# Optimization experiments

Hardware: AMD Instinct MI355X
Metric: run time of the kernel (lower is better)

## Reference

```python
import jax, jax.numpy as jnp
import numpy as np

WS = 2
D = 128  # hidden_dim per direction
SCALE_X = float(np.sqrt(2.0))  # rescale=True, highway_bias=0 -> sqrt(1+exp(0))


def sru_bidir(x, W, wc, b, k):
    """Bidirectional single-layer SRU (sru lib, layer_norm=False, rescale=True).
    x: (L, N, din). Returns (L, N, 2*D)."""
    L, N, _ = x.shape
    U = (x @ W).reshape(L, N, 2, D, k)  # (L,N,dir,D,k)
    vf, vr = wc.reshape(2, 2, D)  # each (dir, D)
    bf, br = b.reshape(2, 2, D)
    # time-reverse the backward direction so one scan handles both
    U = jnp.concatenate([U[:, :, :1], U[::-1, :, 1:]], axis=2)
    if k == 4:
        xprime = U[..., 3]
    else:
        xp = x.reshape(L, N, 2, D)
        xprime = jnp.concatenate([xp[:, :, :1], xp[::-1, :, 1:]], axis=2) * SCALE_X

    def step(c, inp):
        u0, u1, u2, xpt = inp  # each (N,2,D)
        f = jax.nn.sigmoid(u1 + vf * c + bf)
        c = f * c + (1.0 - f) * u0
        r = jax.nn.sigmoid(u2 + vr * c + br)
        h = r * c + (1.0 - r) * xpt
        return c, h

    c0 = jnp.zeros((N, 2, D), dtype=x.dtype)
    _, H = jax.lax.scan(step, c0, (U[..., 0], U[..., 1], U[..., 2], xprime))
    # un-reverse backward direction outputs
    H = jnp.concatenate([H[:, :, :1], H[::-1, :, 1:]], axis=2)
    return H.reshape(L, N, 2 * D)


def setup_inputs() -> dict:
    key = jax.random.key(0)
    ks = jax.random.split(key, 6)
    B, C, Himg, Wimg = 8, 3, 224, 224
    F = WS * WS * C  # 12
    inp = {
        "x": jax.random.normal(ks[0], (B, C, Himg, Wimg), jnp.float32),
        "W1": jax.random.normal(ks[1], (F, 2 * D * 4), jnp.float32) * (1.0 / np.sqrt(F)),
        "wc1": jax.random.normal(ks[2], (2 * 2 * D,), jnp.float32) * 0.1,
        "b1": jnp.zeros((2 * 2 * D,), jnp.float32),
        "W2": jax.random.normal(ks[3], (2 * D, 2 * D * 3), jnp.float32) * (1.0 / np.sqrt(2 * D)),
        "wc2": jax.random.normal(ks[4], (2 * 2 * D,), jnp.float32) * 0.1,
        "b2": jnp.zeros((2 * 2 * D,), jnp.float32),
    }
    return inp


def reference(x, W1, wc1, b1, W2, wc2, b2):
    B, C, Himg, Wimg = x.shape
    Hp, Wp = Himg // WS, Wimg // WS
    F = WS * WS * C
    # get_valid_patches: (B, Hp, Wp, C*ws*ws) with (C, wh, ww) flatten order
    p = x.reshape(B, C, Hp, WS, Wp, WS).transpose(0, 2, 4, 1, 3, 5).reshape(B, Hp, Wp, F)
    # input_array = patches.permute(2,0,3,1) -> (Hp, B, Wp, F)
    # apply_one_direction on firstVRNN: merge Hp into batch, scan over Wp
    a1 = p.transpose(1, 0, 2, 3).reshape(Hp * B, Wp, F).transpose(1, 0, 2)  # (Wp, Hp*B, F)
    h1 = sru_bidir(a1, W1, wc1, b1, k=4)  # (Wp, Hp*B, 2D)
    h1 = h1.transpose(1, 0, 2).reshape(Hp, B, Wp, 2 * D)
    # vertical_results = out.permute(2,1,0,3) -> (Wp, B, Hp, 2D)
    v = h1.transpose(2, 1, 0, 3)
    # second direction: merge Wp into batch, scan over Hp
    a2 = v.reshape(Wp * B, Hp, 2 * D).transpose(1, 0, 2)  # (Hp, Wp*B, 2D)
    h2 = sru_bidir(a2, W2, wc2, b2, k=3)  # (Hp, Wp*B, 2D)
    h2 = h2.transpose(1, 0, 2).reshape(Wp, B, Hp, 2 * D)
    # feature_map.permute(1,3,2,0) -> (B, 2D, Hp, Wp)
    return h2.transpose(1, 3, 2, 0)
```

## Files before the change

### kernel.cpp

```cpp
#include <hip/hip_runtime.h>
#include <hip/hip_bf16.h>

typedef unsigned short ushort_t;
typedef unsigned int uint_t;

typedef __bf16 bf16x8 __attribute__((ext_vector_type(8)));
typedef float f32x4 __attribute__((ext_vector_type(4)));

__device__ __forceinline__ float bf2f(ushort_t u) {
    return __uint_as_float(((uint_t)u) << 16);
}
__device__ __forceinline__ ushort_t f2bf(float f) {
    uint_t x = __float_as_uint(f);
    uint_t r = (x + 0x7FFFu + ((x >> 16) & 1u)) >> 16;
    return (ushort_t)r;
}
__device__ __forceinline__ float sigmoidf_fast(float x) {
    return 1.0f / (1.0f + __expf(-x));
}

#define PP 12544
#define PLANE 25690112ULL

__global__ __launch_bounds__(256) void permute_w2(const float* __restrict__ W2,
                                                  ushort_t* __restrict__ W2t) {
    int i = blockIdx.x * 256 + threadIdx.x;
    int np = i >> 8;
    int k  = i & 255;
    int kk  = np >> 8;
    int rem = np & 255;
    int dir = rem >> 7;
    int d   = rem & 127;
    int oc = dir * 384 + d * 3 + kk;
    W2t[np * 256 + k] = f2bf(W2[k * 768 + oc]);
}

__global__ __launch_bounds__(256) void scan1(const float* __restrict__ x,
                                             const float* __restrict__ W1,
                                             const float* __restrict__ wc1,
                                             const float* __restrict__ b1,
                                             ushort_t* __restrict__ H1a) {
    __shared__ float patch[112 * 12];
    const int n1 = blockIdx.x;
    const int hp = n1 >> 3, b = n1 & 7;
    const int tid = threadIdx.x;

    for (int e = tid; e < 1344; e += 256) {
        int c = e / 448;
        int rem = e % 448;
        int wh = rem / 224;
        int pos = rem % 224;
        float v = x[((b * 3 + c) * 224 + (2 * hp + wh)) * 224 + pos];
        patch[(pos >> 1) * 12 + c * 4 + wh * 2 + (pos & 1)] = v;
    }

    float4 w[12];
    const float4* W1v = (const float4*)W1;
#pragma unroll
    for (int j = 0; j < 12; ++j) w[j] = W1v[j * 256 + tid];

    const float vf = wc1[tid],       vr = wc1[256 + tid];
    const float bfv = b1[tid],       brv = b1[256 + tid];
    const int dir = tid >> 7;

    __syncthreads();

    float cst = 0.0f;
    for (int t = 0; t < 112; ++t) {
        const int tt = dir ? (111 - t) : t;
        const float4* pp = (const float4*)(patch + tt * 12);
        float4 p0 = pp[0], p1 = pp[1], p2 = pp[2];
        float pj[12] = {p0.x, p0.y, p0.z, p0.w, p1.x, p1.y, p1.z, p1.w,
                        p2.x, p2.y, p2.z, p2.w};
        float u0 = 0.f, u1 = 0.f, u2 = 0.f, u3 = 0.f;
#pragma unroll
        for (int j = 0; j < 12; ++j) {
            float pv = pj[j];
            u0 = fmaf(w[j].x, pv, u0);
            u1 = fmaf(w[j].y, pv, u1);
            u2 = fmaf(w[j].z, pv, u2);
            u3 = fmaf(w[j].w, pv, u3);
        }
        float f = sigmoidf_fast(u1 + vf * cst + bfv);
        cst = f * cst + (1.0f - f) * u0;
        float r = sigmoidf_fast(u2 + vr * cst + brv);
        float h = r * cst + (1.0f - r) * u3;
        H1a[((size_t)b * PP + hp * 112 + tt) * 256 + tid] = f2bf(h);
    }
}

__global__ __launch_bounds__(256) void xp_plane(const ushort_t* __restrict__ H1a,
                                                ushort_t* __restrict__ U2t) {
    __shared__ ushort_t tile[64 * 66];
    const int pt = blockIdx.x;
    const int ct = blockIdx.y;
    const int b  = blockIdx.z;
    const int p0 = pt * 64, ch0 = ct * 64;
    const int tid = threadIdx.x;
    const float SCALE_X = 1.41421356237309515f;

#pragma unroll
    for (int rep = 0; rep < 16; ++rep) {
        int idx = rep * 256 + tid;
        int pl = idx >> 6;
        int cl = idx & 63;
        float v = bf2f(H1a[((size_t)b * PP + p0 + pl) * 256 + ch0 + cl]);
        tile[pl * 66 + cl] = f2bf(v * SCALE_X);
    }
    __syncthreads();
#pragma unroll
    for (int rep = 0; rep < 16; ++rep) {
        int idx = rep * 256 + tid;
        int cl = idx >> 6;
        int pl = idx & 63;
        U2t[3 * PLANE + ((size_t)b * 256 + ch0 + cl) * PP + p0 + pl] =
            tile[pl * 66 + cl];
    }
}

__global__ __launch_bounds__(256) void gemm2(const ushort_t* __restrict__ A,
                                             const ushort_t* __restrict__ Bt,
                                             ushort_t* __restrict__ U2t) {
    __shared__ ushort_t As[128 * 32];
    __shared__ ushort_t Bs[128 * 32];
    const int m0 = blockIdx.y * 128;
    const int bb = blockIdx.y / 98;
    const int p0 = (blockIdx.y % 98) * 128;
    const int n0 = blockIdx.x * 128;
    const int kidx = n0 >> 8;
    const int ch0  = n0 & 255;
    const int tid = threadIdx.x;
    const int w = tid >> 6, lane = tid & 63;
    const int wm = w >> 1, wn = w & 1;
    const int lr = lane >> 2;
    const int lc = (lane & 3) * 8;
    const int ln16 = lane & 15;
    const int k8 = (lane >> 4) * 8;

    f32x4 acc[4][4] = {};

    for (int kb = 0; kb < 256; kb += 32) {
        if (kb) __syncthreads();
#pragma unroll
        for (int q = 0; q < 2; ++q) {
            int r = w * 32 + q * 16;
            const ushort_t* gA = A + (size_t)(m0 + r + lr) * 256 + kb + lc;
            __builtin_amdgcn_global_load_lds(
                (const __attribute__((address_space(1))) uint_t*)gA,
                (__attribute__((address_space(3))) uint_t*)(As + r * 32), 16, 0, 0);
            const ushort_t* gB = Bt + (size_t)(n0 + r + lr) * 256 + kb + lc;
            __builtin_amdgcn_global_load_lds(
                (const __attribute__((address_space(1))) uint_t*)gB,
                (__attribute__((address_space(3))) uint_t*)(Bs + r * 32), 16, 0, 0);
        }
        __syncthreads();

        bf16x8 af[4], bf[4];
#pragma unroll
        for (int i = 0; i < 4; ++i) {
            af[i] = *(const bf16x8*)(As + (wm * 64 + i * 16 + ln16) * 32 + k8);
            bf[i] = *(const bf16x8*)(Bs + (wn * 64 + i * 16 + ln16) * 32 + k8);
        }
#pragma unroll
        for (int i = 0; i < 4; ++i)
#pragma unroll
            for (int j = 0; j < 4; ++j)
                acc[i][j] = __builtin_amdgcn_mfma_f32_16x16x32_bf16(
                    af[i], bf[j], acc[i][j], 0, 0, 0);
    }

    const int rq = (lane >> 4) * 4;
    const size_t planeBase = (size_t)kidx * PLANE + (size_t)(bb * 256 + ch0) * PP;
#pragma unroll
    for (int i = 0; i < 4; ++i) {
        int p = p0 + wm * 64 + i * 16 + rq;
#pragma unroll
        for (int j = 0; j < 4; ++j) {
            int ch_l = wn * 64 + j * 16 + ln16;
            ushort4 v;
            v.x = f2bf(acc[i][j][0]);
            v.y = f2bf(acc[i][j][1]);
            v.z = f2bf(acc[i][j][2]);
            v.w = f2bf(acc[i][j][3]);
            *(ushort4*)(U2t + planeBase + (size_t)ch_l * PP + p) = v;
        }
    }
}

__global__ __launch_bounds__(256) void scan2(const ushort_t* __restrict__ U2t,
                                             const float* __restrict__ wc2,
                                             const float* __restrict__ b2,
                                             float* __restrict__ out) {
    const int cb = blockIdx.x;
    const int b  = blockIdx.y;
    const int tid = threadIdx.x;
    const int ch = cb * 2 + (tid >> 7);
    const int wp = tid & 127;
    if (wp >= 112) return;
    const int dir = ch >> 7;

    const float vf = wc2[ch],  vr = wc2[256 + ch];
    const float bfv = b2[ch],  brv = b2[256 + ch];

    const int tt0 = dir ? 111 : 0;
    const long dstep = dir ? -112 : 112;
    const long ostep = dir ? -112 : 112;

    long off  = (long)((size_t)(b * 256 + ch) * PP) + tt0 * 112 + wp;
    long oOff = (long)((size_t)(b * 256 + ch) * 112 + tt0) * 112 + wp;

    const ushort_t* P = U2t;
    ushort_t a0 = P[off];
    ushort_t a1 = P[PLANE + off];
    ushort_t a2 = P[2 * PLANE + off];
    ushort_t a3 = P[3 * PLANE + off];

    float cst = 0.0f;
    for (int t = 0; t < 112; ++t) {
        long noff = off + ((t < 111) ? dstep : 0);
        ushort_t n0 = P[noff];
        ushort_t n1 = P[PLANE + noff];
        ushort_t n2 = P[2 * PLANE + noff];
        ushort_t n3 = P[3 * PLANE + noff];

        float u0 = bf2f(a0), u1 = bf2f(a1), u2v = bf2f(a2);
        float xp = bf2f(a3);
        float f = sigmoidf_fast(u1 + vf * cst + bfv);
        cst = f * cst + (1.0f - f) * u0;
        float r = sigmoidf_fast(u2v + vr * cst + brv);
        out[oOff] = r * cst + (1.0f - r) * xp;

        a0 = n0; a1 = n1; a2 = n2; a3 = n3;
        off = noff;
        oOff += ostep;
    }
}

extern "C" void kernel_launch(void* const* d_in, const int* in_sizes, int n_in,
                              void* d_out, int out_size, void* d_ws, size_t ws_size,
                              hipStream_t stream) {
    const float* x   = (const float*)d_in[0];
    const float* W1  = (const float*)d_in[1];
    const float* wc1 = (const float*)d_in[2];
    const float* b1  = (const float*)d_in[3];
    const float* W2  = (const float*)d_in[4];
    const float* wc2 = (const float*)d_in[5];
    const float* b2  = (const float*)d_in[6];
    float* out = (float*)d_out;

    char* ws = (char*)d_ws;
    ushort_t* H1a = (ushort_t*)(ws);
    ushort_t* U2t = (ushort_t*)(ws + 51380224);
    ushort_t* W2t = (ushort_t*)(ws + 51380224 + 205520896);

    permute_w2<<<768, 256, 0, stream>>>(W2, W2t);
    scan1<<<896, 256, 0, stream>>>(x, W1, wc1, b1, H1a);
    xp_plane<<<dim3(196, 4, 8), 256, 0, stream>>>(H1a, U2t);
    gemm2<<<dim3(6, 784), 256, 0, stream>>>(H1a, W2t, U2t);
    scan2<<<dim3(128, 8), 256, 0, stream>>>(U2t, wc2, b2, out);
}
```

Before: 401.9 us.

## Fuse xprime transpose into scan1, halve gemm2 syncs, deepen scan2 prefetch

The scaled xprime plane is now built inside scan1 via an LDS buffer and transposed store, removing the separate xp_plane kernel and its re-read of H1a. gemm2 loads two 32-wide K slices per barrier, halving synchronisations per tile. scan2 prefetches three steps ahead instead of one to hide global load latency in the serial recurrence. Costs are larger LDS use in scan1, which lowers occupancy, and more registers in scan2.

Result: faster. 380.4 us (-5.4%).

```diff
diff --git a/kernel.cpp b/kernel.cpp
--- a/kernel.cpp
+++ b/kernel.cpp
@@ -39,11 +39,14 @@
                                              const float* __restrict__ W1,
                                              const float* __restrict__ wc1,
                                              const float* __restrict__ b1,
-                                             ushort_t* __restrict__ H1a) {
+                                             ushort_t* __restrict__ H1a,
+                                             ushort_t* __restrict__ U2t) {
     __shared__ float patch[112 * 12];
+    __shared__ ushort_t hbuf[112 * 258];
     const int n1 = blockIdx.x;
     const int hp = n1 >> 3, b = n1 & 7;
     const int tid = threadIdx.x;
+    const float SCALE_X = 1.41421356237309515f;
 
     for (int e = tid; e < 1344; e += 256) {
         int c = e / 448;
@@ -86,43 +89,23 @@
         float r = sigmoidf_fast(u2 + vr * cst + brv);
         float h = r * cst + (1.0f - r) * u3;
         H1a[((size_t)b * PP + hp * 112 + tt) * 256 + tid] = f2bf(h);
-    }
-}
-
-__global__ __launch_bounds__(256) void xp_plane(const ushort_t* __restrict__ H1a,
-                                                ushort_t* __restrict__ U2t) {
-    __shared__ ushort_t tile[64 * 66];
-    const int pt = blockIdx.x;
-    const int ct = blockIdx.y;
-    const int b  = blockIdx.z;
-    const int p0 = pt * 64, ch0 = ct * 64;
-    const int tid = threadIdx.x;
-    const float SCALE_X = 1.41421356237309515f;
-
-#pragma unroll
-    for (int rep = 0; rep < 16; ++rep) {
-        int idx = rep * 256 + tid;
-        int pl = idx >> 6;
-        int cl = idx & 63;
-        float v = bf2f(H1a[((size_t)b * PP + p0 + pl) * 256 + ch0 + cl]);
-        tile[pl * 66 + cl] = f2bf(v * SCALE_X);
-    }
+        hbuf[tt * 258 + tid] = f2bf(h * SCALE_X);
+    }
+
     __syncthreads();
-#pragma unroll
-    for (int rep = 0; rep < 16; ++rep) {
-        int idx = rep * 256 + tid;
-        int cl = idx >> 6;
-        int pl = idx & 63;
-        U2t[3 * PLANE + ((size_t)b * 256 + ch0 + cl) * PP + p0 + pl] =
-            tile[pl * 66 + cl];
+    const size_t base3 = 3 * PLANE + (size_t)b * 256 * PP + (size_t)hp * 112;
+    for (int e = tid; e < 28672; e += 256) {
+        int ch = e / 112;
+        int wp = e - ch * 112;
+        U2t[base3 + (size_t)ch * PP + wp] = hbuf[wp * 258 + ch];
     }
 }
 
 __global__ __launch_bounds__(256) void gemm2(const ushort_t* __restrict__ A,
                                              const ushort_t* __restrict__ Bt,
                                              ushort_t* __restrict__ U2t) {
-    __shared__ ushort_t As[128 * 32];
-    __shared__ ushort_t Bs[128 * 32];
+    __shared__ ushort_t As[2][128 * 32];
+    __shared__ ushort_t Bs[2][128 * 32];
     const int m0 = blockIdx.y * 128;
     const int bb = blockIdx.y / 98;
     const int p0 = (blockIdx.y % 98) * 128;
@@ -139,34 +122,40 @@
 
     f32x4 acc[4][4] = {};
 
-    for (int kb = 0; kb < 256; kb += 32) {
+    for (int kb = 0; kb < 256; kb += 64) {
         if (kb) __syncthreads();
 #pragma unroll
-        for (int q = 0; q < 2; ++q) {
-            int r = w * 32 + q * 16;
-            const ushort_t* gA = A + (size_t)(m0 + r + lr) * 256 + kb + lc;
-            __builtin_amdgcn_global_load_lds(
-                (const __attribute__((address_space(1))) uint_t*)gA,
-                (__attribute__((address_space(3))) uint_t*)(As + r * 32), 16, 0, 0);
-            const ushort_t* gB = Bt + (size_t)(n0 + r + lr) * 256 + kb + lc;
-            __builtin_amdgcn_global_load_lds(
-                (const __attribute__((address_space(1))) uint_t*)gB,
-                (__attribute__((address_space(3))) uint_t*)(Bs + r * 32), 16, 0, 0);
+        for (int h = 0; h < 2; ++h) {
+#pragma unroll
+            for (int q = 0; q < 2; ++q) {
+                int r = w * 32 + q * 16;
+                const ushort_t* gA = A + (size_t)(m0 + r + lr) * 256 + kb + h * 32 + lc;
+                __builtin_amdgcn_global_load_lds(
+                    (const __attribute__((address_space(1))) uint_t*)gA,
+                    (__attribute__((address_space(3))) uint_t*)(As[h] + r * 32), 16, 0, 0);
+                const ushort_t* gB = Bt + (size_t)(n0 + r + lr) * 256 + kb + h * 32 + lc;
+                __builtin_amdgcn_global_load_lds(
+                    (const __attribute__((address_space(1))) uint_t*)gB,
+                    (__attribute__((address_space(3))) uint_t*)(Bs[h] + r * 32), 16, 0, 0);
+            }
         }
         __syncthreads();
 
-        bf16x8 af[4], bf[4];
-#pragma unroll
-        for (int i = 0; i < 4; ++i) {
-            af[i] = *(const bf16x8*)(As + (wm * 64 + i * 16 + ln16) * 32 + k8);
-            bf[i] = *(const bf16x8*)(Bs + (wn * 64 + i * 16 + ln16) * 32 + k8);
-        }
-#pragma unroll
-        for (int i = 0; i < 4; ++i)
-#pragma unroll
-            for (int j = 0; j < 4; ++j)
-                acc[i][j] = __builtin_amdgcn_mfma_f32_16x16x32_bf16(
-                    af[i], bf[j], acc[i][j], 0, 0, 0);
+#pragma unroll
+        for (int h = 0; h < 2; ++h) {
+            bf16x8 af[4], bf[4];
+#pragma unroll
+            for (int i = 0; i < 4; ++i) {
+                af[i] = *(const bf16x8*)(As[h] + (wm * 64 + i * 16 + ln16) * 32 + k8);
+                bf[i] = *(const bf16x8*)(Bs[h] + (wn * 64 + i * 16 + ln16) * 32 + k8);
+            }
+#pragma unroll
+            for (int i = 0; i < 4; ++i)
+#pragma unroll
+                for (int j = 0; j < 4; ++j)
+                    acc[i][j] = __builtin_amdgcn_mfma_f32_16x16x32_bf16(
+                        af[i], bf[j], acc[i][j], 0, 0, 0);
+        }
     }
 
     const int rq = (lane >> 4) * 4;
@@ -206,32 +195,32 @@
     const long dstep = dir ? -112 : 112;
     const long ostep = dir ? -112 : 112;
 
-    long off  = (long)((size_t)(b * 256 + ch) * PP) + tt0 * 112 + wp;
+    const ushort_t* P = U2t;
+    long q    = (long)((size_t)(b * 256 + ch) * PP) + tt0 * 112 + wp;
     long oOff = (long)((size_t)(b * 256 + ch) * 112 + tt0) * 112 + wp;
 
-    const ushort_t* P = U2t;
-    ushort_t a0 = P[off];
-    ushort_t a1 = P[PLANE + off];
-    ushort_t a2 = P[2 * PLANE + off];
-    ushort_t a3 = P[3 * PLANE + off];
+    ushort_t x0 = P[q], x1 = P[PLANE + q], x2 = P[2 * PLANE + q], x3 = P[3 * PLANE + q];
+    q += dstep;
+    ushort_t y0 = P[q], y1 = P[PLANE + q], y2 = P[2 * PLANE + q], y3 = P[3 * PLANE + q];
+    q += dstep;
+    ushort_t z0 = P[q], z1 = P[PLANE + q], z2 = P[2 * PLANE + q], z3 = P[3 * PLANE + q];
 
     float cst = 0.0f;
     for (int t = 0; t < 112; ++t) {
-        long noff = off + ((t < 111) ? dstep : 0);
-        ushort_t n0 = P[noff];
-        ushort_t n1 = P[PLANE + noff];
-        ushort_t n2 = P[2 * PLANE + noff];
-        ushort_t n3 = P[3 * PLANE + noff];
-
-        float u0 = bf2f(a0), u1 = bf2f(a1), u2v = bf2f(a2);
-        float xp = bf2f(a3);
+        long qn = q + ((t < 109) ? dstep : 0);
+        ushort_t w0 = P[qn], w1 = P[PLANE + qn], w2 = P[2 * PLANE + qn], w3 = P[3 * PLANE + qn];
+
+        float u0 = bf2f(x0), u1 = bf2f(x1), u2v = bf2f(x2);
+        float xp = bf2f(x3);
         float f = sigmoidf_fast(u1 + vf * cst + bfv);
         cst = f * cst + (1.0f - f) * u0;
         float r = sigmoidf_fast(u2v + vr * cst + brv);
         out[oOff] = r * cst + (1.0f - r) * xp;
 
-        a0 = n0; a1 = n1; a2 = n2; a3 = n3;
-        off = noff;
+        x0 = y0; x1 = y1; x2 = y2; x3 = y3;
+        y0 = z0; y1 = z1; y2 = z2; y3 = z3;
+        z0 = w0; z1 = w1; z2 = w2; z3 = w3;
+        q = qn;
         oOff += ostep;
     }
 }
@@ -254,8 +243,7 @@
     ushort_t* W2t = (ushort_t*)(ws + 51380224 + 205520896);
 
     permute_w2<<<768, 256, 0, stream>>>(W2, W2t);
-    scan1<<<896, 256, 0, stream>>>(x, W1, wc1, b1, H1a);
-    xp_plane<<<dim3(196, 4, 8), 256, 0, stream>>>(H1a, U2t);
+    scan1<<<896, 256, 0, stream>>>(x, W1, wc1, b1, H1a, U2t);
     gemm2<<<dim3(6, 784), 256, 0, stream>>>(H1a, W2t, U2t);
     scan2<<<dim3(128, 8), 256, 0, stream>>>(U2t, wc2, b2, out);
 }
```
